# Optimization experiments

Measured on AMD Instinct MI355X. Metric: run time of the kernel, lower is better.

## Reference

```python
import jax, jax.numpy as jnp
import numpy as np

N, B, T, D = 6, 4, 1024, 768
P = 3            # number of prior phases
H, Dh = 2, 32    # n_heads, head_dim
I = H * Dh       # inner_dim
EPS = 1e-5


def setup_inputs() -> dict:
    key = jax.random.key(0)
    ks = jax.random.split(key, 9)
    current_states = jax.random.normal(ks[0], (N, B, T, D), dtype=jnp.float32)
    history_states = jax.random.normal(ks[1], (P, N, B, T, D), dtype=jnp.float32)
    attention_mask = jax.random.randint(ks[2], (B, T), 0, 2, dtype=jnp.int32)
    # Linear weights stored as [in, out] (transposed nn.Linear weight)
    s = 1.0 / np.sqrt(D)
    Wq = jax.random.uniform(ks[3], (N, D, I), jnp.float32, -s, s)  # per-domain q proj
    Wk = jax.random.uniform(ks[4], (D, I), jnp.float32, -s, s)     # shared k proj
    Wv = jax.random.uniform(ks[5], (D, I), jnp.float32, -s, s)     # shared v proj
    so = 1.0 / np.sqrt(I)
    Wo = jax.random.uniform(ks[6], (N, I, D), jnp.float32, -so, so)  # per-domain out proj
    gamma = jnp.ones((N, D), jnp.float32)   # per-domain LayerNorm weight
    beta = jnp.zeros((N, D), jnp.float32)   # per-domain LayerNorm bias
    return {"current_states": current_states, "history_states": history_states,
            "attention_mask": attention_mask, "Wq": Wq, "Wk": Wk, "Wv": Wv,
            "Wo": Wo, "gamma": gamma, "beta": beta}


def reference(current_states, history_states, attention_mask, Wq, Wk, Wv, Wo, gamma, beta):
    x = current_states                                   # [N,B,T,D]
    # concat prior phases along time per domain: [N,B,P*T,D]
    prior = jnp.transpose(history_states, (1, 2, 0, 3, 4)).reshape(N, B, P * T, D)

    q = jnp.einsum('nbtd,ndi->nbti', x, Wq).reshape(N, B, T, H, Dh).transpose(0, 1, 3, 2, 4)       # [N,B,H,T,Dh]
    k = jnp.einsum('nbsd,di->nbsi', prior, Wk).reshape(N, B, P * T, H, Dh).transpose(0, 1, 3, 2, 4)  # [N,B,H,S,Dh]
    v = jnp.einsum('nbsd,di->nbsi', prior, Wv).reshape(N, B, P * T, H, Dh).transpose(0, 1, 3, 2, 4)

    scale = 1.0 / jnp.sqrt(jnp.float32(Dh))
    scores = jnp.einsum('nbhtd,nbhsd->nbhts', q, k) * scale  # [N,B,H,T,P*T]
    full_mask = jnp.tile(attention_mask.astype(jnp.float32), (1, P))  # [B,P*T]
    bias = (1.0 - full_mask)[None, :, None, None, :] * -10000.0
    attn = jax.nn.softmax(scores + bias, axis=-1)
    o = jnp.einsum('nbhts,nbhsd->nbhtd', attn, v)            # [N,B,H,T,Dh]
    o = o.transpose(0, 1, 3, 2, 4).reshape(N, B, T, I)       # [N,B,T,I]
    o = jnp.einsum('nbti,nid->nbtd', o, Wo)                  # [N,B,T,D]

    y = x + o  # residual (dropout p=0)
    mu = jnp.mean(y, axis=-1, keepdims=True)
    var = jnp.mean(jnp.square(y - mu), axis=-1, keepdims=True)
    out = (y - mu) * jax.lax.rsqrt(var + EPS)
    out = out * gamma[:, None, None, :] + beta[:, None, None, :]
    return out
```

## Files before the change

### kernel.cpp

```cpp
#include <hip/hip_runtime.h>
#include <hip/hip_bf16.h>
#include <math.h>

#define NDOM 6
#define BB 4
#define TT 1024
#define DD 768
#define PP 3
#define HH 2
#define DHH 32
#define II 64
#define SS (PP*TT)
#define NROW (NDOM*BB*TT)
#define NKVROW (NDOM*BB*SS)
#define NSPLIT 4
#define NKVB (NKVROW/64)
#define NQB  (NROW/64)
#define LNEPS 1e-5f

typedef unsigned int uint;
typedef uint  u32x4  __attribute__((ext_vector_type(4)));
typedef int   i32x2  __attribute__((ext_vector_type(2)));
typedef float f32x2  __attribute__((ext_vector_type(2)));
typedef float f32x4  __attribute__((ext_vector_type(4)));
typedef float f32x16 __attribute__((ext_vector_type(16)));
typedef __bf16 bf16x8 __attribute__((ext_vector_type(8)));

__device__ __forceinline__ f32x16 mfma32(u32x4 a, u32x4 b, f32x16 c) {
  return __builtin_amdgcn_mfma_f32_32x32x16_bf16(
      __builtin_bit_cast(bf16x8, a), __builtin_bit_cast(bf16x8, b), c, 0, 0, 0);
}

__device__ __forceinline__ uint pkbf(float a, float b) {
  union { __bf16 h[2]; uint u; } v;
  v.h[0] = (__bf16)a; v.h[1] = (__bf16)b;
  return v.u;
}
__device__ __forceinline__ float b2f(uint u16) {
  union { uint i; float f; } v; v.i = u16 << 16; return v.f;
}

__device__ __forceinline__ void plswap(uint a, uint b, uint& x, uint& y) {
#if __has_builtin(__builtin_amdgcn_permlane32_swap)
  i32x2 r = __builtin_amdgcn_permlane32_swap((int)a, (int)b, false, false);
  x = (uint)r.x; y = (uint)r.y;
#else
  uint sa = __shfl_xor(a, 32), sb = __shfl_xor(b, 32);
  bool h1 = (threadIdx.x & 32) != 0;
  x = h1 ? sb : a;
  y = h1 ? b : sa;
#endif
}

#if __has_builtin(__builtin_amdgcn_global_load_lds)
#define HAS_GLL 1
typedef __attribute__((address_space(3))) uint lds_u32;
typedef __attribute__((address_space(1))) uint glb_u32;
__device__ __forceinline__ void gload_lds16(const float* src, float* lds_base) {
  __builtin_amdgcn_global_load_lds((const glb_u32*)src, (lds_u32*)lds_base, 16, 0, 0);
}
#else
#define HAS_GLL 0
#endif

__global__ __launch_bounds__(256) void prep_kernel(
    const int* __restrict__ mask, const float* __restrict__ Wk,
    const float* __restrict__ Wv, const float* __restrict__ Wq,
    const float* __restrict__ Wo,
    __hip_bfloat16* __restrict__ Bkv, __hip_bfloat16* __restrict__ Bq,
    __hip_bfloat16* __restrict__ Bo, float* __restrict__ bias2)
{
  int i = blockIdx.x * 256 + threadIdx.x;
  const int N1 = 128 * 768;
  const int N2 = NDOM * 64 * 768;
  const int N3 = NDOM * 768 * 64;
  if (i < N1) {
    int c = i / 768, k = i % 768;
    float v = (c < 64) ? Wk[k * 64 + c] : Wv[k * 64 + (c - 64)];
    Bkv[i] = __float2bfloat16(v);
  } else if (i < N1 + N2) {
    int j = i - N1;
    int n = j / (64 * 768);
    int rem = j % (64 * 768);
    int c = rem / 768, k = rem % 768;
    Bq[j] = __float2bfloat16(Wq[((size_t)n * 768 + k) * 64 + c]);
  } else if (i < N1 + N2 + N3) {
    int j = i - N1 - N2;
    int n = j / (768 * 64);
    int rem = j % (768 * 64);
    int d = rem / 64, k = rem % 64;
    Bo[j] = __float2bfloat16(Wo[((size_t)n * 64 + k) * 768 + d]);
  } else if (i < N1 + N2 + N3 + BB * SS) {
    int j = i - N1 - N2 - N3;
    int b = j / SS, s = j % SS;
    bias2[j] = (1.0f - (float)mask[b * TT + (s & (TT - 1))]) * (-14426.950408889634f);
  }
}

__global__ __launch_bounds__(256, 3) void qkv_gemm_kernel(
    const float* __restrict__ x, const float* __restrict__ hist,
    const __hip_bfloat16* __restrict__ Bkv, const __hip_bfloat16* __restrict__ Bq,
    __hip_bfloat16* __restrict__ Qo, __hip_bfloat16* __restrict__ Kh,
    __hip_bfloat16* __restrict__ Vt2)
{
  __shared__ float As[3][64 * 64];
  const int tid = threadIdx.x;
  const int lane = tid & 63, w = tid >> 6;
  const int cl = lane & 31, hi = lane >> 5;
  const int wr = w >> 1, wc = w & 1;

  const bool isKV = blockIdx.x < NKVB;
  const float* Asrc;
  int nb = 0, s0 = 0, n = 0, brow = 0;
  if (isKV) {
    brow = blockIdx.x * 64;
    nb = brow / SS; n = nb >> 2;
    int b = nb & 3;
    s0 = brow % SS;
    int p = s0 / TT, t0 = s0 % TT;
    Asrc = hist + (((size_t)(p * NDOM + n) * BB + b) * TT + t0) * 768;
  } else {
    brow = (blockIdx.x - NKVB) * 64;
    n = brow >> 12;
    Asrc = x + (size_t)brow * 768;
  }
  const __hip_bfloat16* Bb0 = isKV ? (Bkv + (size_t)(wc * 64 + cl) * 768)
                                   : (Bq + (size_t)n * 64 * 768 + (size_t)(wc * 32 + cl) * 768);
  const __hip_bfloat16* Bb1 = Bkv + (size_t)(wc * 64 + 32 + cl) * 768;

  auto stage = [&](int kk, int buf) {
#pragma unroll
    for (int j = 0; j < 4; ++j) {
      int row = w * 16 + j * 4 + (lane >> 4);
      int gs = (lane & 15) ^ (row & 15);
      const float* src = Asrc + (size_t)row * 768 + kk * 64 + gs * 4;
#if HAS_GLL
      gload_lds16(src, &As[buf][(w * 16 + j * 4) * 64]);
#else
      f32x4 v = *(const f32x4*)src;
      *(f32x4*)(&As[buf][(w * 16 + j * 4) * 64] + lane * 4) = v;
#endif
    }
  };

  u32x4 breg[8];
  auto loadB = [&](int kk) {
#pragma unroll
    for (int ks = 0; ks < 4; ++ks) {
      int kg = kk * 64 + ks * 16 + hi * 8;
      breg[ks] = *(const u32x4*)(Bb0 + kg);
      if (isKV) breg[4 + ks] = *(const u32x4*)(Bb1 + kg);
    }
  };

  f32x16 acc0 = {}, acc1 = {};

  stage(0, 0);
  stage(1, 1);
  loadB(0);
  stage(2, 2);

#pragma unroll
  for (int kk = 0; kk < 12; ++kk) {
    if (kk <= 9) { asm volatile("s_waitcnt vmcnt(4)" ::: "memory"); }
    else         { asm volatile("s_waitcnt vmcnt(0)" ::: "memory"); }
    __builtin_amdgcn_s_barrier();
    {
      const int buf = kk % 3;
      const int row = wr * 32 + cl;
#pragma unroll
      for (int ks = 0; ks < 4; ++ks) {
        int t = ks * 4 + hi * 2;
        int sA = (t ^ (row & 15)) * 4;
        int sB = ((t + 1) ^ (row & 15)) * 4;
        f32x4 a0 = *(const f32x4*)&As[buf][row * 64 + sA];
        f32x4 a1 = *(const f32x4*)&As[buf][row * 64 + sB];
        u32x4 a = {pkbf(a0.x, a0.y), pkbf(a0.z, a0.w), pkbf(a1.x, a1.y), pkbf(a1.z, a1.w)};
        acc0 = mfma32(a, breg[ks], acc0);
        if (isKV) acc1 = mfma32(a, breg[4 + ks], acc1);
      }
    }
    __builtin_amdgcn_s_barrier();
    if (kk + 1 < 12) loadB(kk + 1);
    if (kk + 3 < 12) stage(kk + 3, kk % 3);
  }

  if (isKV) {
    if (wc == 0) {
      const size_t base0 = (size_t)(nb * 2 + 0) * SS;
      const size_t base1 = (size_t)(nb * 2 + 1) * SS;
#pragma unroll
      for (int r = 0; r < 16; ++r) {
        int rl = (r & 3) + 8 * (r >> 2) + 4 * hi;
        int s  = s0 + wr * 32 + rl;
        Kh[(base0 + s) * 32 + cl] = __float2bfloat16(acc0[r]);
        Kh[(base1 + s) * 32 + cl] = __float2bfloat16(acc1[r]);
      }
    } else {
#pragma unroll
      for (int k = 0; k < 4; ++k) {
        int sb = (s0 + wr * 32 + 8 * k) >> 3;
        size_t A0 = (((size_t)(nb * 2 + 0) * (SS / 8) + sb) * 32 + cl) * 8 + 4 * hi;
        size_t A1 = (((size_t)(nb * 2 + 1) * (SS / 8) + sb) * 32 + cl) * 8 + 4 * hi;
        *(uint2*)(Vt2 + A0) = uint2{pkbf(acc0[4*k], acc0[4*k+1]), pkbf(acc0[4*k+2], acc0[4*k+3])};
        *(uint2*)(Vt2 + A1) = uint2{pkbf(acc1[4*k], acc1[4*k+1]), pkbf(acc1[4*k+2], acc1[4*k+3])};
      }
    }
  } else {
#pragma unroll
    for (int r = 0; r < 16; ++r) {
      int rl = (r & 3) + 8 * (r >> 2) + 4 * hi;
      Qo[(size_t)(brow + wr * 32 + rl) * 64 + wc * 32 + cl] = __float2bfloat16(acc0[r]);
    }
  }
}

struct KV { u32x4 k0, k1, k2, k3, v0, v1, v2, v3; };

__global__ __launch_bounds__(256) void attn_kernel(
    const __hip_bfloat16* __restrict__ Q, const __hip_bfloat16* __restrict__ Kh,
    const __hip_bfloat16* __restrict__ Vt2, const float* __restrict__ bias2,
    __hip_bfloat16* __restrict__ Op, float* __restrict__ Mp, float* __restrict__ Lp)
{
  const int tid = threadIdx.x;
  const int lane = tid & 63, w = tid >> 6;
  const int cl = lane & 31, hi = lane >> 5;
  const int bid = blockIdx.x;
  const int g = bid % 48;
  const int rest = bid / 48;
  const int sp = rest >> 3;
  const int tq = rest & 7;
  const int qtile = tq * 4 + w;
  const int h = g & 1, nb = g >> 1;
  const int b = nb & 3;
  const int qrow = nb * TT + qtile * 32;
  const int sbase = sp * (SS / NSPLIT);

  const __hip_bfloat16* Qp = Q + (size_t)(qrow + cl) * 64 + h * 32 + hi * 8;
  u32x4 qf0 = *(const u32x4*)Qp;
  u32x4 qf1 = *(const u32x4*)(Qp + 16);

  const __hip_bfloat16* Kp = Kh + ((size_t)(nb * 2 + h) * SS + sbase) * 32;
  const __hip_bfloat16* Vp = Vt2 + (size_t)(nb * 2 + h) * SS * 32 + (size_t)sbase * 32;
  const float* Bp = bias2 + b * SS + sbase + hi * 4;

  const float scale2 = 0.17677669529663687f * 1.4426950408889634f;
  const f32x2 sc2 = {scale2, scale2};

  f32x16 ot = {};
  float m = -1e30f, lsum = 0.f;

  auto loadKV = [&](int it) {
    KV t;
    const __hip_bfloat16* kp = Kp + (size_t)it * 64 * 32;
    t.k0 = *(const u32x4*)(kp + cl * 32 + hi * 8);
    t.k1 = *(const u32x4*)(kp + cl * 32 + 16 + hi * 8);
    t.k2 = *(const u32x4*)(kp + 1024 + cl * 32 + hi * 8);
    t.k3 = *(const u32x4*)(kp + 1024 + cl * 32 + 16 + hi * 8);
    const __hip_bfloat16* vp = Vp + (size_t)it * 64 * 32;
    t.v0 = *(const u32x4*)(vp + ((0 * 2 + hi) * 32 + cl) * 8);
    t.v1 = *(const u32x4*)(vp + ((1 * 2 + hi) * 32 + cl) * 8);
    t.v2 = *(const u32x4*)(vp + ((2 * 2 + hi) * 32 + cl) * 8);
    t.v3 = *(const u32x4*)(vp + ((3 * 2 + hi) * 32 + cl) * 8);
    return t;
  };

  auto compute = [&](const KV& t, int it) {
    f32x16 pz0 = {}, pz1 = {};
    pz0 = mfma32(t.k0, qf0, pz0);
    pz0 = mfma32(t.k1, qf1, pz0);
    pz1 = mfma32(t.k2, qf0, pz1);
    pz1 = mfma32(t.k3, qf1, pz1);
    const float* bp = Bp + it * 64;
    f32x4 b4[8];
#pragma unroll
    for (int q = 0; q < 8; ++q) b4[q] = *(const f32x4*)(bp + 8 * q);
    f32x2 p2[16];
#pragma unroll
    for (int i = 0; i < 8; ++i) {
      f32x4 bq0 = b4[i >> 1];
      f32x4 bq1 = b4[4 + (i >> 1)];
      f32x2 bv0 = (i & 1) ? f32x2{bq0.z, bq0.w} : f32x2{bq0.x, bq0.y};
      f32x2 bv1 = (i & 1) ? f32x2{bq1.z, bq1.w} : f32x2{bq1.x, bq1.y};
      p2[i]     = f32x2{pz0[2*i], pz0[2*i+1]} * sc2 + bv0;
      p2[8 + i] = f32x2{pz1[2*i], pz1[2*i+1]} * sc2 + bv1;
    }
    f32x2 mx = p2[0];
#pragma unroll
    for (int i = 1; i < 16; ++i) {
      mx.x = fmaxf(mx.x, p2[i].x);
      mx.y = fmaxf(mx.y, p2[i].y);
    }
    float tm = fmaxf(mx.x, mx.y);
    tm = fmaxf(tm, __shfl_xor(tm, 32));
    if (!__all(tm - m <= 8.f)) {
      float mn = fmaxf(m, tm);
      float f = exp2f(m - mn);
#pragma unroll
      for (int i = 0; i < 16; ++i) ot[i] *= f;
      lsum *= f;
      m = mn;
    }
    const f32x2 m2 = {m, m};
    f32x2 s2 = {0.f, 0.f};
#pragma unroll
    for (int i = 0; i < 16; ++i) {
      f32x2 d = p2[i] - m2;
      f32x2 e = {exp2f(d.x), exp2f(d.y)};
      p2[i] = e;
      s2 += e;
    }
    float ts = s2.x + s2.y;
    ts += __shfl_xor(ts, 32);
    lsum += ts;
    uint cv[16];
#pragma unroll
    for (int i = 0; i < 16; ++i) cv[i] = pkbf(p2[i].x, p2[i].y);
    u32x4 pf0, pf1, pf2, pf3;
    {
      uint x0, y0, x1, y1;
      plswap(cv[0], cv[2],  x0, y0); plswap(cv[1], cv[3],  x1, y1);
      pf0 = u32x4{x0, x1, y0, y1};
      plswap(cv[4], cv[6],  x0, y0); plswap(cv[5], cv[7],  x1, y1);
      pf1 = u32x4{x0, x1, y0, y1};
      plswap(cv[8], cv[10], x0, y0); plswap(cv[9], cv[11], x1, y1);
      pf2 = u32x4{x0, x1, y0, y1};
      plswap(cv[12], cv[14], x0, y0); plswap(cv[13], cv[15], x1, y1);
      pf3 = u32x4{x0, x1, y0, y1};
    }
    ot = mfma32(t.v0, pf0, ot);
    ot = mfma32(t.v1, pf1, ot);
    ot = mfma32(t.v2, pf2, ot);
    ot = mfma32(t.v3, pf3, ot);
  };

  KV cur = loadKV(0);
#pragma unroll 1
  for (int it = 0; it < 12; ++it) {
    KV nxt = loadKV(it + 1 < 12 ? it + 1 : 11);
    compute(cur, it);
    cur = nxt;
    __builtin_amdgcn_s_barrier();
  }

  __hip_bfloat16* op = Op + ((size_t)sp * NROW + qrow + cl) * 64 + h * 32 + 4 * hi;
#pragma unroll
  for (int k = 0; k < 4; ++k) {
    uint2 wv = {pkbf(ot[4*k], ot[4*k+1]), pkbf(ot[4*k+2], ot[4*k+3])};
    *(uint2*)(op + 8 * k) = wv;
  }
  if (lane < 32) {
    int mi = ((sp * 24 + nb) * 2 + h) * TT + qtile * 32 + cl;
    Mp[mi] = m;
    Lp[mi] = lsum;
  }
}

__global__ __launch_bounds__(256) void oproj_ln_kernel(
    const float* __restrict__ x, const __hip_bfloat16* __restrict__ Op,
    const float* __restrict__ Mp, const float* __restrict__ Lp,
    const __hip_bfloat16* __restrict__ Bo, const float* __restrict__ gamma,
    const float* __restrict__ beta, float* __restrict__ out)
{
  __shared__ float red[4][32][2];
  __shared__ float redf[32][2];
  const int tid = threadIdx.x;
  const int lane = tid & 63, w = tid >> 6;
  const int cl = lane & 31, hi = lane >> 5;
  const int row0 = blockIdx.x * 32;
  const int n = row0 >> 12;
  const int nb = row0 >> 10;
  const int trow = (row0 & 1023) + cl;
  const int MLS = 24 * 2 * TT;

  float wsp[2][NSPLIT];
#pragma unroll
  for (int h = 0; h < 2; ++h) {
    int mi = (nb * 2 + h) * TT + trow;
    float mv[NSPLIT], lv[NSPLIT];
#pragma unroll
    for (int sp = 0; sp < NSPLIT; ++sp) { mv[sp] = Mp[mi + sp * MLS]; lv[sp] = Lp[mi + sp * MLS]; }
    float ms = mv[0];
#pragma unroll
    for (int sp = 1; sp < NSPLIT; ++sp) ms = fmaxf(ms, mv[sp]);
    float den = 0.f;
#pragma unroll
    for (int sp = 0; sp < NSPLIT; ++sp) { wsp[h][sp] = exp2f(mv[sp] - ms); den = fmaf(lv[sp], wsp[h][sp], den); }
    float inv = 1.0f / den;
#pragma unroll
    for (int sp = 0; sp < NSPLIT; ++sp) wsp[h][sp] *= inv;
  }

  u32x4 af[4];
#pragma unroll
  for (int ks = 0; ks < 4; ++ks) {
    int h = ks >> 1;
    size_t off = (size_t)(row0 + cl) * 64 + ks * 16 + hi * 8;
    f32x2 s0 = {}, s1 = {}, s2 = {}, s3 = {};
#pragma unroll
    for (int sp = 0; sp < NSPLIT; ++sp) {
      u32x4 v = *(const u32x4*)(Op + (size_t)sp * NROW * 64 + off);
      float wv = wsp[h][sp];
      s0 += f32x2{b2f(v[0] & 0xffffu), b2f(v[0] >> 16)} * wv;
      s1 += f32x2{b2f(v[1] & 0xffffu), b2f(v[1] >> 16)} * wv;
      s2 += f32x2{b2f(v[2] & 0xffffu), b2f(v[2] >> 16)} * wv;
      s3 += f32x2{b2f(v[3] & 0xffffu), b2f(v[3] >> 16)} * wv;
    }
    af[ks] = u32x4{pkbf(s0.x, s0.y), pkbf(s1.x, s1.y), pkbf(s2.x, s2.y), pkbf(s3.x, s3.y)};
  }

  const __hip_bfloat16* Bp = Bo + ((size_t)n * 768 + w * 192 + cl) * 64 + hi * 8;
  f32x16 acc[6] = {};
#pragma unroll
  for (int ks = 0; ks < 4; ++ks) {
#pragma unroll
    for (int t = 0; t < 6; ++t) {
      u32x4 bb = *(const u32x4*)(Bp + (size_t)(t * 32) * 64 + ks * 16);
      acc[t] = mfma32(af[ks], bb, acc[t]);
    }
  }

  float s1[16], s2[16];
#pragma unroll
  for (int r = 0; r < 16; ++r) { s1[r] = 0.f; s2[r] = 0.f; }
#pragma unroll
  for (int t = 0; t < 6; ++t) {
#pragma unroll
    for (int r = 0; r < 16; ++r) {
      int R = (r & 3) + 8 * (r >> 2) + 4 * hi;
      int col = w * 192 + t * 32 + cl;
      float y = acc[t][r] + x[(size_t)(row0 + R) * 768 + col];
      acc[t][r] = y;
      s1[r] += y;
      s2[r] = fmaf(y, y, s2[r]);
    }
  }
#pragma unroll
  for (int r = 0; r < 16; ++r) {
#pragma unroll
    for (int off = 1; off < 32; off <<= 1) {
      s1[r] += __shfl_xor(s1[r], off);
      s2[r] += __shfl_xor(s2[r], off);
    }
  }
  if (cl == 0) {
#pragma unroll
    for (int r = 0; r < 16; ++r) {
      int R = (r & 3) + 8 * (r >> 2) + 4 * hi;
      red[w][R][0] = s1[r];
      red[w][R][1] = s2[r];
    }
  }
  __syncthreads();
  if (tid < 64) {
    int R = tid & 31, st = tid >> 5;
    redf[R][st] = red[0][R][st] + red[1][R][st] + red[2][R][st] + red[3][R][st];
  }
  __syncthreads();

  float gv[6], bv[6];
#pragma unroll
  for (int t = 0; t < 6; ++t) {
    int col = w * 192 + t * 32 + cl;
    gv[t] = gamma[n * 768 + col];
    bv[t] = beta[n * 768 + col];
  }
#pragma unroll
  for (int r = 0; r < 16; ++r) {
    int R = (r & 3) + 8 * (r >> 2) + 4 * hi;
    float mu = redf[R][0] * (1.0f / 768.0f);
    float var = redf[R][1] * (1.0f / 768.0f) - mu * mu;
    float rs = rsqrtf(var + LNEPS);
#pragma unroll
    for (int t = 0; t < 6; ++t) {
      int col = w * 192 + t * 32 + cl;
      out[(size_t)(row0 + R) * 768 + col] = (acc[t][r] - mu) * rs * gv[t] + bv[t];
    }
  }
}

extern "C" void kernel_launch(void* const* d_in, const int* in_sizes, int n_in,
                              void* d_out, int out_size, void* d_ws, size_t ws_size,
                              hipStream_t stream) {
  const float* x     = (const float*)d_in[0];
  const float* hist  = (const float*)d_in[1];
  const int*   mask  = (const int*)d_in[2];
  const float* Wq    = (const float*)d_in[3];
  const float* Wk    = (const float*)d_in[4];
  const float* Wv    = (const float*)d_in[5];
  const float* Wo    = (const float*)d_in[6];
  const float* gamma = (const float*)d_in[7];
  const float* beta  = (const float*)d_in[8];
  float* out = (float*)d_out;

  char* ws = (char*)d_ws;
  __hip_bfloat16* Qb  = (__hip_bfloat16*)ws;  ws += (size_t)NROW * II * 2;
  __hip_bfloat16* Kh  = (__hip_bfloat16*)ws;  ws += (size_t)NKVROW * II * 2;
  __hip_bfloat16* Vt2 = (__hip_bfloat16*)ws;  ws += (size_t)NKVROW * II * 2;
  __hip_bfloat16* Op  = (__hip_bfloat16*)ws;  ws += (size_t)NSPLIT * NROW * II * 2;
  float* Mp           = (float*)ws;           ws += (size_t)NSPLIT * 24 * 2 * TT * 4;
  float* Lp           = (float*)ws;           ws += (size_t)NSPLIT * 24 * 2 * TT * 4;
  __hip_bfloat16* Bkv = (__hip_bfloat16*)ws;  ws += (size_t)128 * 768 * 2;
  __hip_bfloat16* Bq  = (__hip_bfloat16*)ws;  ws += (size_t)NDOM * 64 * 768 * 2;
  __hip_bfloat16* Bo  = (__hip_bfloat16*)ws;  ws += (size_t)NDOM * 768 * 64 * 2;
  float* bias2        = (float*)ws;           ws += (size_t)BB * SS * 4;

  const int PREP_N = 128*768 + NDOM*64*768 + NDOM*768*64 + BB*SS;
  prep_kernel<<<(PREP_N + 255) / 256, 256, 0, stream>>>(mask, Wk, Wv, Wq, Wo, Bkv, Bq, Bo, bias2);
  qkv_gemm_kernel<<<NKVB + NQB, 256, 0, stream>>>(x, hist, Bkv, Bq, Qb, Kh, Vt2);
  attn_kernel<<<48 * 8 * NSPLIT, 256, 0, stream>>>(Qb, Kh, Vt2, bias2, Op, Mp, Lp);
  oproj_ln_kernel<<<NROW / 32, 256, 0, stream>>>(x, Op, Mp, Lp, Bo, gamma, beta, out);
}
```

Baseline: 228.8 us.

## Stage swizzled B weights in LDS and double QKV GEMM row tile to 128

The QKV projection GEMM now processes 128 rows per block, and each wave owns 32 rows across all output columns. The B weight tile is staged into LDS via global_load_lds with an XOR swizzle that the prep kernel pre-applies, replacing the earlier per-lane register loads of B. The aim is to cut redundant B traffic and halve the block count. In exchange, the three-stage prefetch pipeline on A is replaced by a single buffer with two syncthreads per k-step, which exposes load latency and may reduce overlap.

```diff
diff --git a/kernel.cpp b/kernel.cpp
--- a/kernel.cpp
+++ b/kernel.cpp
@@ -14,8 +14,8 @@
 #define NROW (NDOM*BB*TT)
 #define NKVROW (NDOM*BB*SS)
 #define NSPLIT 4
-#define NKVB (NKVROW/64)
-#define NQB  (NROW/64)
+#define NKVB (NKVROW/128)
+#define NQB  (NROW/128)
 #define LNEPS 1e-5f
 
 typedef unsigned int uint;
@@ -56,7 +56,7 @@
 #define HAS_GLL 1
 typedef __attribute__((address_space(3))) uint lds_u32;
 typedef __attribute__((address_space(1))) uint glb_u32;
-__device__ __forceinline__ void gload_lds16(const float* src, float* lds_base) {
+__device__ __forceinline__ void gll16(const void* src, void* lds_base) {
   __builtin_amdgcn_global_load_lds((const glb_u32*)src, (lds_u32*)lds_base, 16, 0, 0);
 }
 #else
@@ -75,14 +75,18 @@
   const int N2 = NDOM * 64 * 768;
   const int N3 = NDOM * 768 * 64;
   if (i < N1) {
-    int c = i / 768, k = i % 768;
+    int c = i / 768, kd = i % 768;
+    int e = kd & 7, ud = (kd >> 3) & 7, kk = kd >> 6;
+    int k = (kk << 6) + ((ud ^ (c & 7)) << 3) + e;
     float v = (c < 64) ? Wk[k * 64 + c] : Wv[k * 64 + (c - 64)];
     Bkv[i] = __float2bfloat16(v);
   } else if (i < N1 + N2) {
     int j = i - N1;
     int n = j / (64 * 768);
     int rem = j % (64 * 768);
-    int c = rem / 768, k = rem % 768;
+    int c = rem / 768, kd = rem % 768;
+    int e = kd & 7, ud = (kd >> 3) & 7, kk = kd >> 6;
+    int k = (kk << 6) + ((ud ^ (c & 7)) << 3) + e;
     Bq[j] = __float2bfloat16(Wq[((size_t)n * 768 + k) * 64 + c]);
   } else if (i < N1 + N2 + N3) {
     int j = i - N1 - N2;
@@ -97,120 +101,122 @@
   }
 }
 
-__global__ __launch_bounds__(256, 3) void qkv_gemm_kernel(
+__global__ __launch_bounds__(256) void qkv_gemm_kernel(
     const float* __restrict__ x, const float* __restrict__ hist,
     const __hip_bfloat16* __restrict__ Bkv, const __hip_bfloat16* __restrict__ Bq,
     __hip_bfloat16* __restrict__ Qo, __hip_bfloat16* __restrict__ Kh,
     __hip_bfloat16* __restrict__ Vt2)
 {
-  __shared__ float As[3][64 * 64];
+  __shared__ float As[128 * 64];
+  __shared__ __hip_bfloat16 Bs[128 * 64];
   const int tid = threadIdx.x;
   const int lane = tid & 63, w = tid >> 6;
   const int cl = lane & 31, hi = lane >> 5;
-  const int wr = w >> 1, wc = w & 1;
 
   const bool isKV = blockIdx.x < NKVB;
   const float* Asrc;
   int nb = 0, s0 = 0, n = 0, brow = 0;
   if (isKV) {
-    brow = blockIdx.x * 64;
+    brow = blockIdx.x * 128;
     nb = brow / SS; n = nb >> 2;
     int b = nb & 3;
     s0 = brow % SS;
     int p = s0 / TT, t0 = s0 % TT;
     Asrc = hist + (((size_t)(p * NDOM + n) * BB + b) * TT + t0) * 768;
   } else {
-    brow = (blockIdx.x - NKVB) * 64;
+    brow = (blockIdx.x - NKVB) * 128;
     n = brow >> 12;
     Asrc = x + (size_t)brow * 768;
   }
-  const __hip_bfloat16* Bb0 = isKV ? (Bkv + (size_t)(wc * 64 + cl) * 768)
-                                   : (Bq + (size_t)n * 64 * 768 + (size_t)(wc * 32 + cl) * 768);
-  const __hip_bfloat16* Bb1 = Bkv + (size_t)(wc * 64 + 32 + cl) * 768;
-
-  auto stage = [&](int kk, int buf) {
-#pragma unroll
-    for (int j = 0; j < 4; ++j) {
-      int row = w * 16 + j * 4 + (lane >> 4);
-      int gs = (lane & 15) ^ (row & 15);
+  const __hip_bfloat16* Bsrc = isKV ? Bkv : (Bq + (size_t)n * 64 * 768);
+  const int BROWS = isKV ? 128 : 64;
+  const int NACC = isKV ? 4 : 2;
+
+  f32x16 acc[4] = {};
+
+  const int lrow16 = lane >> 4, lslot16 = lane & 15;
+  const int lrow8  = lane >> 3, lslot8  = lane & 7;
+
+  for (int kk = 0; kk < 12; ++kk) {
+#pragma unroll
+    for (int j = 0; j < 8; ++j) {
+      int row0 = w * 32 + j * 4;
+      int row = row0 + lrow16;
+      int gs = lslot16 ^ (row & 15);
       const float* src = Asrc + (size_t)row * 768 + kk * 64 + gs * 4;
 #if HAS_GLL
-      gload_lds16(src, &As[buf][(w * 16 + j * 4) * 64]);
+      gll16(src, &As[row0 * 64]);
 #else
-      f32x4 v = *(const f32x4*)src;
-      *(f32x4*)(&As[buf][(w * 16 + j * 4) * 64] + lane * 4) = v;
+      *(f32x4*)(&As[row0 * 64] + lane * 4) = *(const f32x4*)src;
 #endif
     }
-  };
-
-  u32x4 breg[8];
-  auto loadB = [&](int kk) {
-#pragma unroll
-    for (int ks = 0; ks < 4; ++ks) {
-      int kg = kk * 64 + ks * 16 + hi * 8;
-      breg[ks] = *(const u32x4*)(Bb0 + kg);
-      if (isKV) breg[4 + ks] = *(const u32x4*)(Bb1 + kg);
-    }
-  };
-
-  f32x16 acc0 = {}, acc1 = {};
-
-  stage(0, 0);
-  stage(1, 1);
-  loadB(0);
-  stage(2, 2);
-
-#pragma unroll
-  for (int kk = 0; kk < 12; ++kk) {
-    if (kk <= 9) { asm volatile("s_waitcnt vmcnt(4)" ::: "memory"); }
-    else         { asm volatile("s_waitcnt vmcnt(0)" ::: "memory"); }
-    __builtin_amdgcn_s_barrier();
     {
-      const int buf = kk % 3;
-      const int row = wr * 32 + cl;
+      int perw = BROWS / 4;
+#pragma unroll
+      for (int j = 0; j < 4; ++j) {
+        if (j * 8 < perw) {
+          int c0 = w * perw + j * 8;
+          int c = c0 + lrow8;
+          const __hip_bfloat16* src = Bsrc + (size_t)c * 768 + kk * 64 + lslot8 * 8;
+#if HAS_GLL
+          gll16(src, &Bs[c0 * 64]);
+#else
+          *(u32x4*)(&Bs[c0 * 64] + lane * 8) = *(const u32x4*)src;
+#endif
+        }
+      }
+    }
+    __syncthreads();
+
+    {
+      const int row = w * 32 + cl;
 #pragma unroll
       for (int ks = 0; ks < 4; ++ks) {
         int t = ks * 4 + hi * 2;
-        int sA = (t ^ (row & 15)) * 4;
-        int sB = ((t + 1) ^ (row & 15)) * 4;
-        f32x4 a0 = *(const f32x4*)&As[buf][row * 64 + sA];
-        f32x4 a1 = *(const f32x4*)&As[buf][row * 64 + sB];
+        f32x4 a0 = *(const f32x4*)&As[row * 64 + ((t       ^ (row & 15)) * 4)];
+        f32x4 a1 = *(const f32x4*)&As[row * 64 + (((t + 1) ^ (row & 15)) * 4)];
         u32x4 a = {pkbf(a0.x, a0.y), pkbf(a0.z, a0.w), pkbf(a1.x, a1.y), pkbf(a1.z, a1.w)};
-        acc0 = mfma32(a, breg[ks], acc0);
-        if (isKV) acc1 = mfma32(a, breg[4 + ks], acc1);
+        int u0 = ks * 2 + hi;
+#pragma unroll
+        for (int g = 0; g < 4; ++g) {
+          if (g < NACC) {
+            int c = g * 32 + cl;
+            u32x4 b = *(const u32x4*)&Bs[c * 64 + ((u0 ^ (c & 7)) * 8)];
+            acc[g] = mfma32(a, b, acc[g]);
+          }
+        }
       }
     }
-    __builtin_amdgcn_s_barrier();
-    if (kk + 1 < 12) loadB(kk + 1);
-    if (kk + 3 < 12) stage(kk + 3, kk % 3);
+    __syncthreads();
   }
 
   if (isKV) {
-    if (wc == 0) {
+    {
       const size_t base0 = (size_t)(nb * 2 + 0) * SS;
       const size_t base1 = (size_t)(nb * 2 + 1) * SS;
 #pragma unroll
       for (int r = 0; r < 16; ++r) {
         int rl = (r & 3) + 8 * (r >> 2) + 4 * hi;
-        int s  = s0 + wr * 32 + rl;
-        Kh[(base0 + s) * 32 + cl] = __float2bfloat16(acc0[r]);
-        Kh[(base1 + s) * 32 + cl] = __float2bfloat16(acc1[r]);
+        int s  = s0 + w * 32 + rl;
+        Kh[(base0 + s) * 32 + cl] = __float2bfloat16(acc[0][r]);
+        Kh[(base1 + s) * 32 + cl] = __float2bfloat16(acc[1][r]);
       }
-    } else {
-#pragma unroll
-      for (int k = 0; k < 4; ++k) {
-        int sb = (s0 + wr * 32 + 8 * k) >> 3;
-        size_t A0 = (((size_t)(nb * 2 + 0) * (SS / 8) + sb) * 32 + cl) * 8 + 4 * hi;
-        size_t A1 = (((size_t)(nb * 2 + 1) * (SS / 8) + sb) * 32 + cl) * 8 + 4 * hi;
-        *(uint2*)(Vt2 + A0) = uint2{pkbf(acc0[4*k], acc0[4*k+1]), pkbf(acc0[4*k+2], acc0[4*k+3])};
-        *(uint2*)(Vt2 + A1) = uint2{pkbf(acc1[4*k], acc1[4*k+1]), pkbf(acc1[4*k+2], acc1[4*k+3])};
-      }
+    }
+#pragma unroll
+    for (int k = 0; k < 4; ++k) {
+      int sb = (s0 + w * 32 + 8 * k) >> 3;
+      size_t A0 = (((size_t)(nb * 2 + 0) * (SS / 8) + sb) * 32 + cl) * 8 + 4 * hi;
+      size_t A1 = (((size_t)(nb * 2 + 1) * (SS / 8) + sb) * 32 + cl) * 8 + 4 * hi;
+      *(uint2*)(Vt2 + A0) = uint2{pkbf(acc[2][4*k], acc[2][4*k+1]), pkbf(acc[2][4*k+2], acc[2][4*k+3])};
+      *(uint2*)(Vt2 + A1) = uint2{pkbf(acc[3][4*k], acc[3][4*k+1]), pkbf(acc[3][4*k+2], acc[3][4*k+3])};
     }
   } else {
 #pragma unroll
     for (int r = 0; r < 16; ++r) {
       int rl = (r & 3) + 8 * (r >> 2) + 4 * hi;
-      Qo[(size_t)(brow + wr * 32 + rl) * 64 + wc * 32 + cl] = __float2bfloat16(acc0[r]);
+      size_t rb = (size_t)(brow + w * 32 + rl) * 64;
+      Qo[rb + cl]      = __float2bfloat16(acc[0][r]);
+      Qo[rb + 32 + cl] = __float2bfloat16(acc[1][r]);
     }
   }
 }
```

After: 201.6 us. 1.14x faster.
